# Kernel tuning notes

Hardware: AMD Instinct MI355X
Metric: run time of the kernel (lower is better)

Reference implementation:

```python
import jax, jax.numpy as jnp
import numpy as np

EPS = 1e-8

def _gelu(x):
    return jax.nn.gelu(x, approximate=False)  # torch F.gelu default (erf)

def _film_pool(feat, q, film_w, film_b, hid_w, hid_b, fin_w, fin_b):
    # feat: (B,C,H,W), q: (B,Q,E)
    B, C, H, W = feat.shape
    f = feat.reshape(B, C, H * W).transpose(0, 2, 1)            # (B,HW,C)
    gb = q @ film_w + film_b                                    # (B,Q,2C)
    gamma, beta = jnp.split(gb, 2, axis=-1)                     # (B,Q,C) each
    mod = gamma[:, :, None, :] * f[:, None, :, :] + beta[:, :, None, :]  # (B,Q,HW,C)
    h = _gelu(mod @ hid_w + hid_b)                              # (B,Q,HW,Hh)
    attn = jax.nn.sigmoid(h @ fin_w + fin_b)                    # (B,Q,HW,1)
    pooled = (attn * mod).sum(axis=2) / (attn.sum(axis=2) + EPS)  # (B,Q,C)
    return pooled, attn[..., 0]                                 # attn map (B,Q,HW)

def setup_inputs() -> dict:
    key = jax.random.key(0)
    ks = jax.random.split(key, 32)
    B, Q, E, Hh = 2, 32, 768, 128
    chans = [64, 128, 256]
    hws = [(80, 80), (40, 40), (20, 20)]
    d = {}
    d['feat0'] = jax.random.normal(ks[0], (B, chans[0], *hws[0]), jnp.float32)
    d['feat1'] = jax.random.normal(ks[1], (B, chans[1], *hws[1]), jnp.float32)
    d['feat2'] = jax.random.normal(ks[2], (B, chans[2], *hws[2]), jnp.float32)
    d['fact_embeddings'] = jax.random.normal(ks[3], (B, Q, E), jnp.float32)
    for i, C in enumerate(chans):
        d[f'film_w{i}'] = jax.random.normal(ks[4 + 4 * i], (E, 2 * C), jnp.float32) * 0.02
        d[f'film_b{i}'] = jnp.zeros((2 * C,), jnp.float32)
        d[f'hid_w{i}'] = jax.random.normal(ks[5 + 4 * i], (C, Hh), jnp.float32) * 0.05
        d[f'hid_b{i}'] = jnp.zeros((Hh,), jnp.float32)
        d[f'fin_w{i}'] = jax.random.normal(ks[6 + 4 * i], (Hh, 1), jnp.float32) * 0.05
        d[f'fin_b{i}'] = jnp.zeros((1,), jnp.float32)
    in_dim = sum(chans) + hws[-1][0] * hws[-1][1]  # 448 + 400 = 848
    d['mlp_w1'] = jax.random.normal(ks[20], (in_dim, 512), jnp.float32) * 0.02
    d['mlp_b1'] = jnp.zeros((512,), jnp.float32)
    d['mlp_w2'] = jax.random.normal(ks[21], (512, 256), jnp.float32) * 0.02
    d['mlp_b2'] = jnp.zeros((256,), jnp.float32)
    d['mlp_w3'] = jax.random.normal(ks[22], (256, 1), jnp.float32) * 0.02
    d['mlp_b3'] = jnp.zeros((1,), jnp.float32)
    return d

def reference(feat0, feat1, feat2, fact_embeddings,
              film_w0, film_b0, hid_w0, hid_b0, fin_w0, fin_b0,
              film_w1, film_b1, hid_w1, hid_b1, fin_w1, fin_b1,
              film_w2, film_b2, hid_w2, hid_b2, fin_w2, fin_b2,
              mlp_w1, mlp_b1, mlp_w2, mlp_b2, mlp_w3, mlp_b3):
    q = fact_embeddings
    p0, _ = _film_pool(feat0, q, film_w0, film_b0, hid_w0, hid_b0, fin_w0, fin_b0)
    p1, _ = _film_pool(feat1, q, film_w1, film_b1, hid_w1, hid_b1, fin_w1, fin_b1)
    p2, a2 = _film_pool(feat2, q, film_w2, film_b2, hid_w2, hid_b2, fin_w2, fin_b2)
    cat = jnp.concatenate([p0, p1, p2, a2], axis=2)  # (B,Q,848)
    x = _gelu(cat @ mlp_w1 + mlp_b1)
    x = _gelu(x @ mlp_w2 + mlp_b2)
    logits = (x @ mlp_w3 + mlp_b3)[..., 0]  # (B,Q)
    return logits
```

## Files before the change

kernel.cpp:

```cpp
#include <hip/hip_runtime.h>
#include <math.h>

#define BQ 64
#define HH 128
#define EPS 1e-8f

typedef short bf16x8 __attribute__((ext_vector_type(8)));
typedef float f32x4  __attribute__((ext_vector_type(4)));

__device__ __forceinline__ float gelu_exact(float x) {
    return 0.5f * x * (1.0f + erff(x * 0.70710678118654752440f));
}

__device__ __forceinline__ unsigned bf16_rne(float x) {
    unsigned u = __float_as_uint(x);
    return (u + 0x7FFFu + ((u >> 16) & 1u)) >> 16;
}
__device__ __forceinline__ uint2 split_pack(float a, float b) {
    unsigned ha = bf16_rne(a);
    float fa = __uint_as_float(ha << 16);
    unsigned la = bf16_rne(a - fa);
    unsigned hb = bf16_rne(b);
    float fb = __uint_as_float(hb << 16);
    unsigned lb = bf16_rne(b - fb);
    uint2 r; r.x = ha | (hb << 16); r.y = la | (lb << 16);
    return r;
}

__device__ __forceinline__
void pack_feat_body(int i,
                    const float* __restrict__ f0, const float* __restrict__ f1,
                    const float* __restrict__ f2,
                    unsigned short* __restrict__ p0h, unsigned short* __restrict__ p0l,
                    unsigned short* __restrict__ p1h, unsigned short* __restrict__ p1l,
                    unsigned short* __restrict__ p2h, unsigned short* __restrict__ p2l)
{
    const float* f; unsigned short *oh, *ol; int HW; int idx;
    if (i < 102400)      { f = f0; oh = p0h; ol = p0l; HW = 6400; idx = i; }
    else if (i < 153600) { f = f1; oh = p1h; ol = p1l; HW = 1600; idx = i - 102400; }
    else if (i < 179200) { f = f2; oh = p2h; ol = p2l; HW = 400;  idx = i - 153600; }
    else return;
    const int px = idx % HW;
    const int cgb = idx / HW;
    const float* src = f + ((size_t)cgb * 8) * HW + px;
    float a[8];
    #pragma unroll
    for (int k = 0; k < 8; ++k) a[k] = src[(size_t)k * HW];
    unsigned hwd[4], lwd[4];
    #pragma unroll
    for (int k = 0; k < 4; ++k) {
        uint2 p = split_pack(a[2 * k], a[2 * k + 1]);
        hwd[k] = p.x; lwd[k] = p.y;
    }
    *(uint4*)&oh[(size_t)idx * 8] = make_uint4(hwd[0], hwd[1], hwd[2], hwd[3]);
    *(uint4*)&ol[(size_t)idx * 8] = make_uint4(lwd[0], lwd[1], lwd[2], lwd[3]);
}

__global__ __launch_bounds__(256)
void prep1_kernel(const float* __restrict__ f0, const float* __restrict__ f1,
                  const float* __restrict__ f2,
                  unsigned short* __restrict__ p0h, unsigned short* __restrict__ p0l,
                  unsigned short* __restrict__ p1h, unsigned short* __restrict__ p1l,
                  unsigned short* __restrict__ p2h, unsigned short* __restrict__ p2l,
                  const float* __restrict__ qe,
                  const float* __restrict__ fw0, const float* __restrict__ fb0,
                  const float* __restrict__ fw1, const float* __restrict__ fb1,
                  const float* __restrict__ fw2, const float* __restrict__ fb2,
                  float* __restrict__ gb0, float* __restrict__ gb1, float* __restrict__ gb2)
{
    const int tid = threadIdx.x;
    if (blockIdx.x < 700) {
        pack_feat_body(blockIdx.x * 256 + tid, f0, f1, f2, p0h, p0l, p1h, p1l, p2h, p2l);
        return;
    }
    __shared__ float sq[768];
    __shared__ float sP[256];
    const int bb = blockIdx.x - 700;
    const int chunk = bb >> 6, bq = bb & 63;
    int s, o0;
    if (chunk == 0)      { s = 0; o0 = 0; }
    else if (chunk <= 2) { s = 1; o0 = (chunk - 1) * 128; }
    else                 { s = 2; o0 = (chunk - 3) * 128; }
    const float* fw  = s == 0 ? fw0 : s == 1 ? fw1 : fw2;
    const float* fbv = s == 0 ? fb0 : s == 1 ? fb1 : fb2;
    float* gb        = s == 0 ? gb0 : s == 1 ? gb1 : gb2;
    const int twoC = 128 << s;

    for (int i = tid; i < 768; i += 256) sq[i] = qe[bq * 768 + i];
    __syncthreads();
    const int o = o0 + (tid & 127), half = tid >> 7;
    const int e0 = half * 384;
    float a0 = 0.f, a1 = 0.f;
    #pragma unroll 2
    for (int e = 0; e < 384; e += 2) {
        a0 = fmaf(sq[e0 + e],     fw[(e0 + e) * twoC + o],     a0);
        a1 = fmaf(sq[e0 + e + 1], fw[(e0 + e + 1) * twoC + o], a1);
    }
    sP[tid] = a0 + a1;
    __syncthreads();
    if (tid < 128) {
        int oo = o0 + tid;
        gb[bq * twoC + oo] = sP[tid] + sP[tid + 128] + fbv[oo];
    }
}

__global__ __launch_bounds__(256)
void prep2_kernel(const float* __restrict__ gb0, const float* __restrict__ gb1,
                  const float* __restrict__ gb2,
                  const float* __restrict__ hw0_, const float* __restrict__ hb0,
                  const float* __restrict__ hw1_, const float* __restrict__ hb1,
                  const float* __restrict__ hw2_, const float* __restrict__ hb2,
                  unsigned short* __restrict__ g0h, unsigned short* __restrict__ g0l,
                  unsigned short* __restrict__ g1h, unsigned short* __restrict__ g1l,
                  unsigned short* __restrict__ g2h, unsigned short* __restrict__ g2l,
                  float* __restrict__ b20, float* __restrict__ b21, float* __restrict__ b22)
{
    const int tid = threadIdx.x;
    if (blockIdx.x < 1792) {
        int i = blockIdx.x * 256 + tid;
        const float *gb, *hw; unsigned short *oh, *ol; int C, idx;
        if (i < 65536)       { gb = gb0; hw = hw0_; oh = g0h; ol = g0l; C = 64;  idx = i; }
        else if (i < 196608) { gb = gb1; hw = hw1_; oh = g1h; ol = g1l; C = 128; idx = i - 65536; }
        else                 { gb = gb2; hw = hw2_; oh = g2h; ol = g2l; C = 256; idx = i - 196608; }
        const int j  = idx & 127;
        const int cg = (idx >> 7) % (C / 8);
        const int bq = idx / (128 * (C / 8));
        const int c0 = cg * 8;
        const float* g = gb + bq * 2 * C;
        float a[8];
        #pragma unroll
        for (int k = 0; k < 8; ++k) a[k] = g[c0 + k] * hw[(size_t)(c0 + k) * HH + j];
        unsigned hwd[4], lwd[4];
        #pragma unroll
        for (int k = 0; k < 4; ++k) {
            uint2 p = split_pack(a[2 * k], a[2 * k + 1]);
            hwd[k] = p.x; lwd[k] = p.y;
        }
        *(uint4*)&oh[(size_t)idx * 8] = make_uint4(hwd[0], hwd[1], hwd[2], hwd[3]);
        *(uint4*)&ol[(size_t)idx * 8] = make_uint4(lwd[0], lwd[1], lwd[2], lwd[3]);
        return;
    }
    __shared__ float sBeta[256];
    __shared__ float sP[256];
    const int bb = blockIdx.x - 1792;
    const int s = bb >> 6, bq = bb & 63;
    const float* gb = s == 0 ? gb0 : s == 1 ? gb1 : gb2;
    const float* hw = s == 0 ? hw0_ : s == 1 ? hw1_ : hw2_;
    const float* hb = s == 0 ? hb0 : s == 1 ? hb1 : hb2;
    float* b2       = s == 0 ? b20 : s == 1 ? b21 : b22;
    const int C = 64 << s;

    for (int i = tid; i < C; i += 256) sBeta[i] = gb[bq * 2 * C + C + i];
    __syncthreads();
    const int j = tid & 127, half = tid >> 7;
    const int c0 = half * (C / 2);
    float acc = 0.f;
    for (int c = 0; c < C / 2; ++c)
        acc = fmaf(sBeta[c0 + c], hw[(c0 + c) * HH + j], acc);
    sP[tid] = acc;
    __syncthreads();
    if (tid < 128) b2[bq * HH + tid] = hb[tid] + sP[tid] + sP[tid + 128];
}

#define MFMA3(ACC, ALO, AHI, BH, BL)                                            \
    ACC = __builtin_amdgcn_mfma_f32_16x16x32_bf16(ALO, BH, ACC, 0, 0, 0);       \
    ACC = __builtin_amdgcn_mfma_f32_16x16x32_bf16(AHI, BL, ACC, 0, 0, 0);       \
    ACC = __builtin_amdgcn_mfma_f32_16x16x32_bf16(AHI, BH, ACC, 0, 0, 0);

template<int C, bool WRITE_ATTN>
__device__ __forceinline__
void pool_body(const float* __restrict__ feat, int HW,
               const unsigned short* __restrict__ fh, const unsigned short* __restrict__ fl,
               const unsigned short* __restrict__ gwh, const unsigned short* __restrict__ gwl,
               const float* __restrict__ b2, const float* __restrict__ finw,
               const float* __restrict__ finb,
               float* __restrict__ Sout, float* __restrict__ attn_out,
               int b, int qp, int tile,
               unsigned short* sB, float* sAttn)
{
    const int tid  = threadIdx.x;
    const int w    = tid >> 6;
    const int lane = tid & 63;
    const int l15  = lane & 15, l4 = lane >> 4;
    const int px0  = tile * 256;
    constexpr int CG = C / 8;
    const int bq0 = b * 32 + qp * 2;
    const int bq1 = bq0 + 1;
    const float* fbase = feat + (size_t)b * C * HW;

    f32x4 accA[2][8], accB[2][8];
    #pragma unroll
    for (int jt = 0; jt < 8; ++jt) {
        float bv0 = b2[bq0 * HH + jt * 16 + l15];
        float bv1 = b2[bq1 * HH + jt * 16 + l15];
        accA[0][jt] = (f32x4){bv0, bv0, bv0, bv0};
        accA[1][jt] = (f32x4){bv0, bv0, bv0, bv0};
        accB[0][jt] = (f32x4){bv1, bv1, bv1, bv1};
        accB[1][jt] = (f32x4){bv1, bv1, bv1, bv1};
    }

    const int apx0 = min(px0 + (w * 2 + 0) * 16 + l15, HW - 1);
    const int apx1 = min(px0 + (w * 2 + 1) * 16 + l15, HW - 1);
    const unsigned short* fhp = fh + (size_t)b * CG * HW * 8;
    const unsigned short* flp = fl + (size_t)b * CG * HW * 8;
    const unsigned short* q0h = gwh + (size_t)bq0 * CG * 128 * 8;
    const unsigned short* q0l = gwl + (size_t)bq0 * CG * 128 * 8;
    const unsigned short* q1h = gwh + (size_t)bq1 * CG * 128 * 8;
    const unsigned short* q1l = gwl + (size_t)bq1 * CG * 128 * 8;

    for (int ks = 0; ks < CG / 4; ++ks) {
        const size_t arow = (size_t)(ks * 4 + l4) * HW;
        const bf16x8 Ahi0 = *(const bf16x8*)(fhp + (arow + apx0) * 8);
        const bf16x8 Alo0 = *(const bf16x8*)(flp + (arow + apx0) * 8);
        const bf16x8 Ahi1 = *(const bf16x8*)(fhp + (arow + apx1) * 8);
        const bf16x8 Alo1 = *(const bf16x8*)(flp + (arow + apx1) * 8);
        {
            uint4* dst = (uint4*)sB;
            dst[tid]        = ((const uint4*)(q0h + (size_t)ks * 4096))[tid];
            dst[512  + tid] = ((const uint4*)(q0l + (size_t)ks * 4096))[tid];
            dst[1024 + tid] = ((const uint4*)(q1h + (size_t)ks * 4096))[tid];
            dst[1536 + tid] = ((const uint4*)(q1l + (size_t)ks * 4096))[tid];
        }
        __syncthreads();
        const int bofs = (l4 * 128 + l15) * 8;
        #pragma unroll
        for (int jt = 0; jt < 8; ++jt) {
            const bf16x8 B0h = *(const bf16x8*)(sB + bofs + jt * 128);
            const bf16x8 B0l = *(const bf16x8*)(sB + 4096 + bofs + jt * 128);
            MFMA3(accA[0][jt], Alo0, Ahi0, B0h, B0l)
            MFMA3(accA[1][jt], Alo1, Ahi1, B0h, B0l)
            const bf16x8 B1h = *(const bf16x8*)(sB + 8192 + bofs + jt * 128);
            const bf16x8 B1l = *(const bf16x8*)(sB + 12288 + bofs + jt * 128);
            MFMA3(accB[0][jt], Alo0, Ahi0, B1h, B1l)
            MFMA3(accB[1][jt], Alo1, Ahi1, B1h, B1l)
        }
        __syncthreads();
    }

    const float fb0 = finb[0];
    #pragma unroll
    for (int pt = 0; pt < 2; ++pt) {
        float p0[4] = {0.f, 0.f, 0.f, 0.f};
        float p1[4] = {0.f, 0.f, 0.f, 0.f};
        #pragma unroll
        for (int jt = 0; jt < 8; ++jt) {
            float fwv = finw[jt * 16 + l15];
            #pragma unroll
            for (int r = 0; r < 4; ++r) {
                p0[r] = fmaf(gelu_exact(accA[pt][jt][r]), fwv, p0[r]);
                p1[r] = fmaf(gelu_exact(accB[pt][jt][r]), fwv, p1[r]);
            }
        }
        #pragma unroll
        for (int r = 0; r < 4; ++r) {
            p0[r] += __shfl_xor(p0[r], 1);  p1[r] += __shfl_xor(p1[r], 1);
            p0[r] += __shfl_xor(p0[r], 2);  p1[r] += __shfl_xor(p1[r], 2);
            p0[r] += __shfl_xor(p0[r], 4);  p1[r] += __shfl_xor(p1[r], 4);
            p0[r] += __shfl_xor(p0[r], 8);  p1[r] += __shfl_xor(p1[r], 8);
        }
        if (l15 == 0) {
            #pragma unroll
            for (int r = 0; r < 4; ++r) {
                int lpx = (w * 2 + pt) * 16 + l4 * 4 + r;
                int px  = px0 + lpx;
                float a0v = (px < HW) ? 1.0f / (1.0f + expf(-(p0[r] + fb0))) : 0.0f;
                float a1v = (px < HW) ? 1.0f / (1.0f + expf(-(p1[r] + fb0))) : 0.0f;
                sAttn[lpx]       = a0v;
                sAttn[256 + lpx] = a1v;
                if (WRITE_ATTN && px < HW) {
                    attn_out[bq0 * HW + px] = a0v;
                    attn_out[bq1 * HW + px] = a1v;
                }
            }
        }
    }
    __syncthreads();

    {
        float sa = sAttn[tid];
        #pragma unroll
        for (int d = 1; d < 64; d <<= 1) sa += __shfl_xor(sa, d);
        if (lane == 0) {
            int bqx = (tid < 256) ? bq0 : bq1;
            atomicAdd(&Sout[bqx * (C + 1) + C], sa);
        }
    }

    constexpr int CPW = C / 8;
    #pragma unroll 1
    for (int ci = 0; ci < CPW; ++ci) {
        const int c2 = w * CPW + ci;
        const float* fr = fbase + (size_t)c2 * HW;
        float s0 = 0.f, s1 = 0.f;
        #pragma unroll
        for (int k = 0; k < 4; ++k) {
            int lpx = lane + 64 * k;
            int gc = min(px0 + lpx, HW - 1);
            float fv = fr[gc];
            s0 = fmaf(fv, sAttn[lpx], s0);
            s1 = fmaf(fv, sAttn[256 + lpx], s1);
        }
        #pragma unroll
        for (int d = 1; d < 64; d <<= 1) {
            s0 += __shfl_xor(s0, d);
            s1 += __shfl_xor(s1, d);
        }
        if (lane == 0) {
            atomicAdd(&Sout[bq0 * (C + 1) + c2], s0);
            atomicAdd(&Sout[bq1 * (C + 1) + c2], s1);
        }
    }
}

__global__ __launch_bounds__(512)
void pool_fused(const unsigned short* __restrict__ f0h, const unsigned short* __restrict__ f0l,
                const unsigned short* __restrict__ f1h, const unsigned short* __restrict__ f1l,
                const unsigned short* __restrict__ f2h, const unsigned short* __restrict__ f2l,
                const unsigned short* __restrict__ g0h, const unsigned short* __restrict__ g0l,
                const unsigned short* __restrict__ g1h, const unsigned short* __restrict__ g1l,
                const unsigned short* __restrict__ g2h, const unsigned short* __restrict__ g2l,
                const float* __restrict__ feat0, const float* __restrict__ feat1,
                const float* __restrict__ feat2,
                const float* __restrict__ b20, const float* __restrict__ b21,
                const float* __restrict__ b22,
                const float* __restrict__ finw0, const float* __restrict__ finb0,
                const float* __restrict__ finw1, const float* __restrict__ finb1,
                const float* __restrict__ finw2, const float* __restrict__ finb2,
                float* __restrict__ S0, float* __restrict__ S1, float* __restrict__ S2,
                float* __restrict__ attn2)
{
    __shared__ __align__(16) unsigned short sB[16384];
    __shared__ float sAttn[512];
    const int blk = blockIdx.x;
    if (blk < 64) {
        int bt = blk >> 4, qp = blk & 15;
        int b = bt >> 1, t = bt & 1;
        pool_body<256, true>(feat2, 400, f2h, f2l, g2h, g2l, b22, finw2, finb2,
                             S2, attn2, b, qp, t, sB, sAttn);
    } else if (blk < 288) {
        int bb = blk - 64; int bt = bb >> 4, qp = bb & 15;
        int b = bt / 7, t = bt % 7;
        pool_body<128, false>(feat1, 1600, f1h, f1l, g1h, g1l, b21, finw1, finb1,
                              S1, nullptr, b, qp, t, sB, sAttn);
    } else {
        int bb = blk - 288; int bt = bb >> 4, qp = bb & 15;
        int b = bt / 25, t = bt % 25;
        pool_body<64, false>(feat0, 6400, f0h, f0l, g0h, g0l, b20, finw0, finb0,
                             S0, nullptr, b, qp, t, sB, sAttn);
    }
}

__global__ __launch_bounds__(256)
void mlp1_kernel(const float* __restrict__ S0, const float* __restrict__ S1,
                 const float* __restrict__ S2,
                 const float* __restrict__ gb0, const float* __restrict__ gb1,
                 const float* __restrict__ gb2,
                 const float* __restrict__ attn2,
                 const float* __restrict__ w1, const float* __restrict__ b1,
                 float* __restrict__ X1)
{
    __shared__ float sCat[848];
    __shared__ float sP[256];
    const int tid = threadIdx.x, bq = blockIdx.x;

    for (int i = tid; i < 448; i += 256) {
        int sc, c;
        if (i < 64)       { sc = 0; c = i; }
        else if (i < 192) { sc = 1; c = i - 64; }
        else              { sc = 2; c = i - 192; }
        const int C = 64 << sc;
        const float* So = (sc == 0) ? S0 : (sc == 1) ? S1 : S2;
        const float* g  = (sc == 0) ? gb0 : (sc == 1) ? gb1 : gb2;
        float Sa = So[bq * (C + 1) + C];
        float Sf = So[bq * (C + 1) + c];
        float gamma = g[bq * 2 * C + c];
        float beta  = g[bq * 2 * C + C + c];
        sCat[i] = (gamma * Sf + beta * Sa) / (Sa + EPS);
    }
    for (int i = tid; i < 400; i += 256) sCat[448 + i] = attn2[bq * 400 + i];
    __syncthreads();

    const int o = blockIdx.y * 128 + (tid & 127), half = tid >> 7;
    const int k0 = half * 424;
    float a0 = 0.f, a1 = 0.f;
    #pragma unroll 2
    for (int k = 0; k < 424; k += 2) {
        a0 = fmaf(sCat[k0 + k],     w1[(k0 + k) * 512 + o],     a0);
        a1 = fmaf(sCat[k0 + k + 1], w1[(k0 + k + 1) * 512 + o], a1);
    }
    sP[tid] = a0 + a1;
    __syncthreads();
    if (tid < 128) {
        int oo = blockIdx.y * 128 + tid;
        X1[bq * 512 + oo] = sP[tid] + sP[tid + 128] + b1[oo];
    }
}

__global__ __launch_bounds__(256)
void mlp23_kernel(const float* __restrict__ X1,
                  const float* __restrict__ w2, const float* __restrict__ b2,
                  const float* __restrict__ w3, const float* __restrict__ b3,
                  float* __restrict__ out)
{
    __shared__ float sX1[512];
    __shared__ float sX2[256];
    __shared__ float sR[4];
    const int tid = threadIdx.x, bq = blockIdx.x;
    for (int i = tid; i < 512; i += 256) sX1[i] = gelu_exact(X1[bq * 512 + i]);
    __syncthreads();
    float a0 = b2[tid], a1 = 0.f, a2 = 0.f, a3 = 0.f;
    #pragma unroll 4
    for (int k = 0; k < 512; k += 4) {
        a0 = fmaf(sX1[k],     w2[(k)     * 256 + tid], a0);
        a1 = fmaf(sX1[k + 1], w2[(k + 1) * 256 + tid], a1);
        a2 = fmaf(sX1[k + 2], w2[(k + 2) * 256 + tid], a2);
        a3 = fmaf(sX1[k + 3], w2[(k + 3) * 256 + tid], a3);
    }
    sX2[tid] = gelu_exact((a0 + a1) + (a2 + a3));
    __syncthreads();
    float p = sX2[tid] * w3[tid];
    #pragma unroll
    for (int d = 1; d < 64; d <<= 1) p += __shfl_xor(p, d);
    if ((tid & 63) == 0) sR[tid >> 6] = p;
    __syncthreads();
    if (tid == 0) out[bq] = sR[0] + sR[1] + sR[2] + sR[3] + b3[0];
}

extern "C" void kernel_launch(void* const* d_in, const int* in_sizes, int n_in,
                              void* d_out, int out_size, void* d_ws, size_t ws_size,
                              hipStream_t stream)
{
    const float* feat0 = (const float*)d_in[0];
    const float* feat1 = (const float*)d_in[1];
    const float* feat2 = (const float*)d_in[2];
    const float* qe    = (const float*)d_in[3];
    const float* film_w0 = (const float*)d_in[4];
    const float* film_b0 = (const float*)d_in[5];
    const float* hid_w0  = (const float*)d_in[6];
    const float* hid_b0  = (const float*)d_in[7];
    const float* fin_w0  = (const float*)d_in[8];
    const float* fin_b0  = (const float*)d_in[9];
    const float* film_w1 = (const float*)d_in[10];
    const float* film_b1 = (const float*)d_in[11];
    const float* hid_w1  = (const float*)d_in[12];
    const float* hid_b1  = (const float*)d_in[13];
    const float* fin_w1  = (const float*)d_in[14];
    const float* fin_b1  = (const float*)d_in[15];
    const float* film_w2 = (const float*)d_in[16];
    const float* film_b2 = (const float*)d_in[17];
    const float* hid_w2  = (const float*)d_in[18];
    const float* hid_b2  = (const float*)d_in[19];
    const float* fin_w2  = (const float*)d_in[20];
    const float* fin_b2  = (const float*)d_in[21];
    const float* mlp_w1  = (const float*)d_in[22];
    const float* mlp_b1  = (const float*)d_in[23];
    const float* mlp_w2  = (const float*)d_in[24];
    const float* mlp_b2  = (const float*)d_in[25];
    const float* mlp_w3  = (const float*)d_in[26];
    const float* mlp_b3  = (const float*)d_in[27];

    float* ws = (float*)d_ws;
    float* S0    = ws;
    float* S1    = ws + 4160;
    float* S2    = ws + 12416;
    float* gb0   = ws + 28864;
    float* gb1   = ws + 37056;
    float* gb2   = ws + 53440;
    float* b20   = ws + 86208;
    float* b21   = ws + 94400;
    float* b22   = ws + 102592;
    float* attn2 = ws + 110784;
    float* X1    = ws + 136384;

    unsigned short* us = (unsigned short*)(ws + 169216);
    unsigned short* f0h = us;
    unsigned short* f0l = f0h + 819200;
    unsigned short* f1h = f0l + 819200;
    unsigned short* f1l = f1h + 409600;
    unsigned short* f2h = f1l + 409600;
    unsigned short* f2l = f2h + 204800;
    unsigned short* g0h = f2l + 204800;
    unsigned short* g0l = g0h + 524288;
    unsigned short* g1h = g0l + 524288;
    unsigned short* g1l = g1h + 1048576;
    unsigned short* g2h = g1l + 1048576;
    unsigned short* g2l = g2h + 2097152;

    hipMemsetAsync(d_ws, 0, 28864 * sizeof(float), stream);

    prep1_kernel<<<1148, 256, 0, stream>>>(
        feat0, feat1, feat2, f0h, f0l, f1h, f1l, f2h, f2l,
        qe, film_w0, film_b0, film_w1, film_b1, film_w2, film_b2,
        gb0, gb1, gb2);

    prep2_kernel<<<1984, 256, 0, stream>>>(
        gb0, gb1, gb2,
        hid_w0, hid_b0, hid_w1, hid_b1, hid_w2, hid_b2,
        g0h, g0l, g1h, g1l, g2h, g2l,
        b20, b21, b22);

    pool_fused<<<1088, 512, 0, stream>>>(
        f0h, f0l, f1h, f1l, f2h, f2l,
        g0h, g0l, g1h, g1l, g2h, g2l,
        feat0, feat1, feat2,
        b20, b21, b22,
        fin_w0, fin_b0, fin_w1, fin_b1, fin_w2, fin_b2,
        S0, S1, S2, attn2);

    mlp1_kernel<<<dim3(BQ, 4), 256, 0, stream>>>(
        S0, S1, S2, gb0, gb1, gb2, attn2, mlp_w1, mlp_b1, X1);

    mlp23_kernel<<<BQ, 256, 0, stream>>>(
        X1, mlp_w2, mlp_b2, mlp_w3, mlp_b3, (float*)d_out);
}
```

Before: 233.8 us.

## Double-buffer FiLM weight tiles via direct global-to-LDS loads and XCD-aware block mapping

```diff
diff --git a/kernel.cpp b/kernel.cpp
--- a/kernel.cpp
+++ b/kernel.cpp
@@ -7,6 +7,9 @@
 
 typedef short bf16x8 __attribute__((ext_vector_type(8)));
 typedef float f32x4  __attribute__((ext_vector_type(4)));
+
+typedef const __attribute__((address_space(1))) void* gptr_t;
+typedef __attribute__((address_space(3))) void* lptr_t;
 
 __device__ __forceinline__ float gelu_exact(float x) {
     return 0.5f * x * (1.0f + erff(x * 0.70710678118654752440f));
@@ -183,7 +186,8 @@
     const int lane = tid & 63;
     const int l15  = lane & 15, l4 = lane >> 4;
     const int px0  = tile * 256;
-    constexpr int CG = C / 8;
+    constexpr int CG  = C / 8;
+    constexpr int NKS = CG / 4;
     const int bq0 = b * 32 + qp * 2;
     const int bq1 = bq0 + 1;
     const float* fbase = feat + (size_t)b * C * HW;
@@ -203,39 +207,53 @@
     const int apx1 = min(px0 + (w * 2 + 1) * 16 + l15, HW - 1);
     const unsigned short* fhp = fh + (size_t)b * CG * HW * 8;
     const unsigned short* flp = fl + (size_t)b * CG * HW * 8;
-    const unsigned short* q0h = gwh + (size_t)bq0 * CG * 128 * 8;
-    const unsigned short* q0l = gwl + (size_t)bq0 * CG * 128 * 8;
-    const unsigned short* q1h = gwh + (size_t)bq1 * CG * 128 * 8;
-    const unsigned short* q1l = gwl + (size_t)bq1 * CG * 128 * 8;
-
-    for (int ks = 0; ks < CG / 4; ++ks) {
+    const unsigned short* qsrc0 = gwh + (size_t)bq0 * CG * 1024;
+    const unsigned short* qsrc1 = gwl + (size_t)bq0 * CG * 1024;
+    const unsigned short* qsrc2 = gwh + (size_t)bq1 * CG * 1024;
+    const unsigned short* qsrc3 = gwl + (size_t)bq1 * CG * 1024;
+
+    const int lane8 = lane * 8;
+    const int woff  = __builtin_amdgcn_readfirstlane(w * 512);
+
+    #define STAGE(KS, BUF)                                                       \
+    {                                                                            \
+        const unsigned short* s0 = qsrc0 + (size_t)(KS) * 4096 + woff + lane8;   \
+        const unsigned short* s1 = qsrc1 + (size_t)(KS) * 4096 + woff + lane8;   \
+        const unsigned short* s2 = qsrc2 + (size_t)(KS) * 4096 + woff + lane8;   \
+        const unsigned short* s3 = qsrc3 + (size_t)(KS) * 4096 + woff + lane8;   \
+        __builtin_amdgcn_global_load_lds((gptr_t)s0, (lptr_t)((BUF) + 0    + woff), 16, 0, 0); \
+        __builtin_amdgcn_global_load_lds((gptr_t)s1, (lptr_t)((BUF) + 4096 + woff), 16, 0, 0); \
+        __builtin_amdgcn_global_load_lds((gptr_t)s2, (lptr_t)((BUF) + 8192 + woff), 16, 0, 0); \
+        __builtin_amdgcn_global_load_lds((gptr_t)s3, (lptr_t)((BUF) + 12288 + woff), 16, 0, 0); \
+    }
+
+    STAGE(0, sB)
+
+    for (int ks = 0; ks < NKS; ++ks) {
+        __syncthreads();
+        unsigned short* cur = sB + (ks & 1) * 16384;
+        if (ks + 1 < NKS) STAGE(ks + 1, sB + (((ks + 1) & 1) * 16384))
+
         const size_t arow = (size_t)(ks * 4 + l4) * HW;
         const bf16x8 Ahi0 = *(const bf16x8*)(fhp + (arow + apx0) * 8);
         const bf16x8 Alo0 = *(const bf16x8*)(flp + (arow + apx0) * 8);
         const bf16x8 Ahi1 = *(const bf16x8*)(fhp + (arow + apx1) * 8);
         const bf16x8 Alo1 = *(const bf16x8*)(flp + (arow + apx1) * 8);
-        {
-            uint4* dst = (uint4*)sB;
-            dst[tid]        = ((const uint4*)(q0h + (size_t)ks * 4096))[tid];
-            dst[512  + tid] = ((const uint4*)(q0l + (size_t)ks * 4096))[tid];
-            dst[1024 + tid] = ((const uint4*)(q1h + (size_t)ks * 4096))[tid];
-            dst[1536 + tid] = ((const uint4*)(q1l + (size_t)ks * 4096))[tid];
-        }
-        __syncthreads();
+
         const int bofs = (l4 * 128 + l15) * 8;
         #pragma unroll
         for (int jt = 0; jt < 8; ++jt) {
-            const bf16x8 B0h = *(const bf16x8*)(sB + bofs + jt * 128);
-            const bf16x8 B0l = *(const bf16x8*)(sB + 4096 + bofs + jt * 128);
+            const bf16x8 B0h = *(const bf16x8*)(cur + bofs + jt * 128);
+            const bf16x8 B0l = *(const bf16x8*)(cur + 4096 + bofs + jt * 128);
             MFMA3(accA[0][jt], Alo0, Ahi0, B0h, B0l)
             MFMA3(accA[1][jt], Alo1, Ahi1, B0h, B0l)
-            const bf16x8 B1h = *(const bf16x8*)(sB + 8192 + bofs + jt * 128);
-            const bf16x8 B1l = *(const bf16x8*)(sB + 12288 + bofs + jt * 128);
+            const bf16x8 B1h = *(const bf16x8*)(cur + 8192 + bofs + jt * 128);
+            const bf16x8 B1l = *(const bf16x8*)(cur + 12288 + bofs + jt * 128);
             MFMA3(accB[0][jt], Alo0, Ahi0, B1h, B1l)
             MFMA3(accB[1][jt], Alo1, Ahi1, B1h, B1l)
         }
-        __syncthreads();
-    }
+    }
+    #undef STAGE
 
     const float fb0 = finb[0];
     #pragma unroll
@@ -329,22 +347,26 @@
                 float* __restrict__ S0, float* __restrict__ S1, float* __restrict__ S2,
                 float* __restrict__ attn2)
 {
-    __shared__ __align__(16) unsigned short sB[16384];
-    __shared__ float sAttn[512];
-    const int blk = blockIdx.x;
-    if (blk < 64) {
-        int bt = blk >> 4, qp = blk & 15;
-        int b = bt >> 1, t = bt & 1;
+    __shared__ __align__(16) unsigned short sB[32768];
+    float* sAttn = (float*)sB;
+
+    const int blk0 = blockIdx.x;
+    const int xcd = blk0 & 7, s = blk0 >> 3;
+    int k, t;
+    if (s < 8)       { k = s >> 1;            t = s & 1; }
+    else if (s < 36) { k = 4 + (s - 8) / 7;   t = (s - 8) % 7; }
+    else             { k = 8 + (s - 36) / 25; t = (s - 36) % 25; }
+    const int b  = xcd >> 2;
+    const int qp = (k & 3) * 4 + (xcd & 3);
+    const int sidx = k >> 2;
+
+    if (sidx == 0) {
         pool_body<256, true>(feat2, 400, f2h, f2l, g2h, g2l, b22, finw2, finb2,
                              S2, attn2, b, qp, t, sB, sAttn);
-    } else if (blk < 288) {
-        int bb = blk - 64; int bt = bb >> 4, qp = bb & 15;
-        int b = bt / 7, t = bt % 7;
+    } else if (sidx == 1) {
         pool_body<128, false>(feat1, 1600, f1h, f1l, g1h, g1l, b21, finw1, finb1,
                               S1, nullptr, b, qp, t, sB, sAttn);
     } else {
-        int bb = blk - 288; int bt = bb >> 4, qp = bb & 15;
-        int b = bt / 25, t = bt % 25;
         pool_body<64, false>(feat0, 6400, f0h, f0l, g0h, g0l, b20, finw0, finb0,
                              S0, nullptr, b, qp, t, sB, sAttn);
     }
```

Result: slower. 246.7 us (+5.5%).

## Stage full per-query weights in LDS once and loop pixel tiles per block

Applied to the files above, without the earlier changes.

```diff
diff --git a/kernel.cpp b/kernel.cpp
--- a/kernel.cpp
+++ b/kernel.cpp
@@ -25,6 +25,9 @@
     unsigned lb = bf16_rne(b - fb);
     uint2 r; r.x = ha | (hb << 16); r.y = la | (lb << 16);
     return r;
+}
+__device__ __forceinline__ float bf_to_f(unsigned short u) {
+    return __uint_as_float((unsigned)u << 16);
 }
 
 __device__ __forceinline__
@@ -66,11 +69,17 @@
                   const float* __restrict__ fw0, const float* __restrict__ fb0,
                   const float* __restrict__ fw1, const float* __restrict__ fb1,
                   const float* __restrict__ fw2, const float* __restrict__ fb2,
-                  float* __restrict__ gb0, float* __restrict__ gb1, float* __restrict__ gb2)
+                  float* __restrict__ gb0, float* __restrict__ gb1, float* __restrict__ gb2,
+                  float* __restrict__ zws)
 {
     const int tid = threadIdx.x;
     if (blockIdx.x < 700) {
         pack_feat_body(blockIdx.x * 256 + tid, f0, f1, f2, p0h, p0l, p1h, p1l, p2h, p2l);
+        return;
+    }
+    if (blockIdx.x >= 1148) {
+        int idx = (blockIdx.x - 1148) * 256 + tid;
+        if (idx < 28864) zws[idx] = 0.0f;
         return;
     }
     __shared__ float sq[768];
@@ -167,148 +176,175 @@
     ACC = __builtin_amdgcn_mfma_f32_16x16x32_bf16(AHI, BL, ACC, 0, 0, 0);       \
     ACC = __builtin_amdgcn_mfma_f32_16x16x32_bf16(AHI, BH, ACC, 0, 0, 0);
 
-template<int C, bool WRITE_ATTN>
+template<int C, int QF, bool WRITE_ATTN>
 __device__ __forceinline__
-void pool_body(const float* __restrict__ feat, int HW,
+void pool_body(int HW,
                const unsigned short* __restrict__ fh, const unsigned short* __restrict__ fl,
                const unsigned short* __restrict__ gwh, const unsigned short* __restrict__ gwl,
                const float* __restrict__ b2, const float* __restrict__ finw,
                const float* __restrict__ finb,
                float* __restrict__ Sout, float* __restrict__ attn_out,
-               int b, int qp, int tile,
+               int b, int qidx, int t0, int nt,
                unsigned short* sB, float* sAttn)
 {
     const int tid  = threadIdx.x;
     const int w    = tid >> 6;
     const int lane = tid & 63;
     const int l15  = lane & 15, l4 = lane >> 4;
-    const int px0  = tile * 256;
-    constexpr int CG = C / 8;
-    const int bq0 = b * 32 + qp * 2;
+    constexpr int CG   = C / 8;
+    constexpr int NKS  = CG / 4;
+    constexpr int SLAB = QF * 8192;
+    const int bq0 = b * 32 + qidx * QF;
     const int bq1 = bq0 + 1;
-    const float* fbase = feat + (size_t)b * C * HW;
-
-    f32x4 accA[2][8], accB[2][8];
-    #pragma unroll
-    for (int jt = 0; jt < 8; ++jt) {
-        float bv0 = b2[bq0 * HH + jt * 16 + l15];
-        float bv1 = b2[bq1 * HH + jt * 16 + l15];
-        accA[0][jt] = (f32x4){bv0, bv0, bv0, bv0};
-        accA[1][jt] = (f32x4){bv0, bv0, bv0, bv0};
-        accB[0][jt] = (f32x4){bv1, bv1, bv1, bv1};
-        accB[1][jt] = (f32x4){bv1, bv1, bv1, bv1};
-    }
-
-    const int apx0 = min(px0 + (w * 2 + 0) * 16 + l15, HW - 1);
-    const int apx1 = min(px0 + (w * 2 + 1) * 16 + l15, HW - 1);
+
     const unsigned short* fhp = fh + (size_t)b * CG * HW * 8;
     const unsigned short* flp = fl + (size_t)b * CG * HW * 8;
-    const unsigned short* q0h = gwh + (size_t)bq0 * CG * 128 * 8;
-    const unsigned short* q0l = gwl + (size_t)bq0 * CG * 128 * 8;
-    const unsigned short* q1h = gwh + (size_t)bq1 * CG * 128 * 8;
-    const unsigned short* q1l = gwl + (size_t)bq1 * CG * 128 * 8;
-
-    for (int ks = 0; ks < CG / 4; ++ks) {
-        const size_t arow = (size_t)(ks * 4 + l4) * HW;
-        const bf16x8 Ahi0 = *(const bf16x8*)(fhp + (arow + apx0) * 8);
-        const bf16x8 Alo0 = *(const bf16x8*)(flp + (arow + apx0) * 8);
-        const bf16x8 Ahi1 = *(const bf16x8*)(fhp + (arow + apx1) * 8);
-        const bf16x8 Alo1 = *(const bf16x8*)(flp + (arow + apx1) * 8);
-        {
-            uint4* dst = (uint4*)sB;
-            dst[tid]        = ((const uint4*)(q0h + (size_t)ks * 4096))[tid];
-            dst[512  + tid] = ((const uint4*)(q0l + (size_t)ks * 4096))[tid];
-            dst[1024 + tid] = ((const uint4*)(q1h + (size_t)ks * 4096))[tid];
-            dst[1536 + tid] = ((const uint4*)(q1l + (size_t)ks * 4096))[tid];
-        }
-        __syncthreads();
-        const int bofs = (l4 * 128 + l15) * 8;
+
+    {
+        const unsigned short* srcs[4];
+        srcs[0] = gwh + (size_t)bq0 * CG * 1024;
+        srcs[1] = gwl + (size_t)bq0 * CG * 1024;
+        if (QF == 2) {
+            srcs[2] = gwh + (size_t)bq1 * CG * 1024;
+            srcs[3] = gwl + (size_t)bq1 * CG * 1024;
+        }
+        #pragma unroll
+        for (int ks = 0; ks < NKS; ++ks) {
+            #pragma unroll
+            for (int p = 0; p < 2 * QF; ++p) {
+                const uint4* s = (const uint4*)(srcs[p] + (size_t)ks * 4096);
+                uint4* d = (uint4*)(sB + ks * SLAB + p * 4096);
+                d[tid] = s[tid];
+            }
+        }
+    }
+    __syncthreads();
+
+    const float fb0 = finb[0];
+
+    for (int ti = 0; ti < nt; ++ti) {
+        const int tile = t0 + ti;
+        const int px0  = tile * 256;
+        const int apx0 = min(px0 + (w * 2 + 0) * 16 + l15, HW - 1);
+        const int apx1 = min(px0 + (w * 2 + 1) * 16 + l15, HW - 1);
+
+        f32x4 accA[2][8], accB[2][8];
         #pragma unroll
         for (int jt = 0; jt < 8; ++jt) {
-            const bf16x8 B0h = *(const bf16x8*)(sB + bofs + jt * 128);
-            const bf16x8 B0l = *(const bf16x8*)(sB + 4096 + bofs + jt * 128);
-            MFMA3(accA[0][jt], Alo0, Ahi0, B0h, B0l)
-            MFMA3(accA[1][jt], Alo1, Ahi1, B0h, B0l)
-            const bf16x8 B1h = *(const bf16x8*)(sB + 8192 + bofs + jt * 128);
-            const bf16x8 B1l = *(const bf16x8*)(sB + 12288 + bofs + jt * 128);
-            MFMA3(accB[0][jt], Alo0, Ahi0, B1h, B1l)
-            MFMA3(accB[1][jt], Alo1, Ahi1, B1h, B1l)
+            float bv0 = b2[bq0 * HH + jt * 16 + l15];
+            accA[0][jt] = (f32x4){bv0, bv0, bv0, bv0};
+            accA[1][jt] = (f32x4){bv0, bv0, bv0, bv0};
+            if (QF == 2) {
+                float bv1 = b2[bq1 * HH + jt * 16 + l15];
+                accB[0][jt] = (f32x4){bv1, bv1, bv1, bv1};
+                accB[1][jt] = (f32x4){bv1, bv1, bv1, bv1};
+            }
+        }
+
+        #pragma unroll 2
+        for (int ks = 0; ks < NKS; ++ks) {
+            const size_t ar = (size_t)(ks * 4 + l4) * HW;
+            const bf16x8 Ahi0 = *(const bf16x8*)(fhp + (ar + apx0) * 8);
+            const bf16x8 Alo0 = *(const bf16x8*)(flp + (ar + apx0) * 8);
+            const bf16x8 Ahi1 = *(const bf16x8*)(fhp + (ar + apx1) * 8);
+            const bf16x8 Alo1 = *(const bf16x8*)(flp + (ar + apx1) * 8);
+            const unsigned short* S = sB + ks * SLAB;
+            const int bofs = (l4 * 128 + l15) * 8;
+            #pragma unroll
+            for (int jt = 0; jt < 8; ++jt) {
+                const bf16x8 B0h = *(const bf16x8*)(S + bofs + jt * 128);
+                const bf16x8 B0l = *(const bf16x8*)(S + 4096 + bofs + jt * 128);
+                MFMA3(accA[0][jt], Alo0, Ahi0, B0h, B0l)
+                MFMA3(accA[1][jt], Alo1, Ahi1, B0h, B0l)
+                if (QF == 2) {
+                    const bf16x8 B1h = *(const bf16x8*)(S + 8192 + bofs + jt * 128);
+                    const bf16x8 B1l = *(const bf16x8*)(S + 12288 + bofs + jt * 128);
+                    MFMA3(accB[0][jt], Alo0, Ahi0, B1h, B1l)
+                    MFMA3(accB[1][jt], Alo1, Ahi1, B1h, B1l)
+                }
+            }
+        }
+
+        #pragma unroll
+        for (int pt = 0; pt < 2; ++pt) {
+            float p0[4] = {0.f, 0.f, 0.f, 0.f};
+            float p1[4] = {0.f, 0.f, 0.f, 0.f};
+            #pragma unroll
+            for (int jt = 0; jt < 8; ++jt) {
+                float fwv = finw[jt * 16 + l15];
+                #pragma unroll
+                for (int r = 0; r < 4; ++r) {
+                    p0[r] = fmaf(gelu_exact(accA[pt][jt][r]), fwv, p0[r]);
+                    if (QF == 2) p1[r] = fmaf(gelu_exact(accB[pt][jt][r]), fwv, p1[r]);
+                }
+            }
+            #pragma unroll
+            for (int r = 0; r < 4; ++r) {
+                p0[r] += __shfl_xor(p0[r], 1);
+                p0[r] += __shfl_xor(p0[r], 2);
+                p0[r] += __shfl_xor(p0[r], 4);
+                p0[r] += __shfl_xor(p0[r], 8);
+                if (QF == 2) {
+                    p1[r] += __shfl_xor(p1[r], 1);
+                    p1[r] += __shfl_xor(p1[r], 2);
+                    p1[r] += __shfl_xor(p1[r], 4);
+                    p1[r] += __shfl_xor(p1[r], 8);
+                }
+            }
+            if (l15 == 0) {
+                #pragma unroll
+                for (int r = 0; r < 4; ++r) {
+                    int lpx = (w * 2 + pt) * 16 + l4 * 4 + r;
+                    int px  = px0 + lpx;
+                    float a0v = (px < HW) ? 1.0f / (1.0f + expf(-(p0[r] + fb0))) : 0.0f;
+                    sAttn[lpx] = a0v;
+                    if (WRITE_ATTN && px < HW) attn_out[bq0 * HW + px] = a0v;
+                    if (QF == 2) {
+                        float a1v = (px < HW) ? 1.0f / (1.0f + expf(-(p1[r] + fb0))) : 0.0f;
+                        sAttn[256 + lpx] = a1v;
+                        if (WRITE_ATTN && px < HW) attn_out[bq1 * HW + px] = a1v;
+                    }
+                }
+            }
         }
         __syncthreads();
-    }
-
-    const float fb0 = finb[0];
-    #pragma unroll
-    for (int pt = 0; pt < 2; ++pt) {
-        float p0[4] = {0.f, 0.f, 0.f, 0.f};
-        float p1[4] = {0.f, 0.f, 0.f, 0.f};
-        #pragma unroll
-        for (int jt = 0; jt < 8; ++jt) {
-            float fwv = finw[jt * 16 + l15];
-            #pragma unroll
-            for (int r = 0; r < 4; ++r) {
-                p0[r] = fmaf(gelu_exact(accA[pt][jt][r]), fwv, p0[r]);
-                p1[r] = fmaf(gelu_exact(accB[pt][jt][r]), fwv, p1[r]);
-            }
-        }
-        #pragma unroll
-        for (int r = 0; r < 4; ++r) {
-            p0[r] += __shfl_xor(p0[r], 1);  p1[r] += __shfl_xor(p1[r], 1);
-            p0[r] += __shfl_xor(p0[r], 2);  p1[r] += __shfl_xor(p1[r], 2);
-            p0[r] += __shfl_xor(p0[r], 4);  p1[r] += __shfl_xor(p1[r], 4);
-            p0[r] += __shfl_xor(p0[r], 8);  p1[r] += __shfl_xor(p1[r], 8);
-        }
-        if (l15 == 0) {
-            #pragma unroll
-            for (int r = 0; r < 4; ++r) {
-                int lpx = (w * 2 + pt) * 16 + l4 * 4 + r;
-                int px  = px0 + lpx;
-                float a0v = (px < HW) ? 1.0f / (1.0f + expf(-(p0[r] + fb0))) : 0.0f;
-                float a1v = (px < HW) ? 1.0f / (1.0f + expf(-(p1[r] + fb0))) : 0.0f;
-                sAttn[lpx]       = a0v;
-                sAttn[256 + lpx] = a1v;
-                if (WRITE_ATTN && px < HW) {
-                    attn_out[bq0 * HW + px] = a0v;
-                    attn_out[bq1 * HW + px] = a1v;
-                }
-            }
-        }
-    }
-    __syncthreads();
-
-    {
-        float sa = sAttn[tid];
-        #pragma unroll
-        for (int d = 1; d < 64; d <<= 1) sa += __shfl_xor(sa, d);
-        if (lane == 0) {
-            int bqx = (tid < 256) ? bq0 : bq1;
-            atomicAdd(&Sout[bqx * (C + 1) + C], sa);
-        }
-    }
-
-    constexpr int CPW = C / 8;
-    #pragma unroll 1
-    for (int ci = 0; ci < CPW; ++ci) {
-        const int c2 = w * CPW + ci;
-        const float* fr = fbase + (size_t)c2 * HW;
-        float s0 = 0.f, s1 = 0.f;
-        #pragma unroll
-        for (int k = 0; k < 4; ++k) {
-            int lpx = lane + 64 * k;
-            int gc = min(px0 + lpx, HW - 1);
-            float fv = fr[gc];
-            s0 = fmaf(fv, sAttn[lpx], s0);
-            s1 = fmaf(fv, sAttn[256 + lpx], s1);
-        }
-        #pragma unroll
-        for (int d = 1; d < 64; d <<= 1) {
-            s0 += __shfl_xor(s0, d);
-            s1 += __shfl_xor(s1, d);
-        }
-        if (lane == 0) {
-            atomicAdd(&Sout[bq0 * (C + 1) + c2], s0);
-            atomicAdd(&Sout[bq1 * (C + 1) + c2], s1);
-        }
+
+        if (QF == 2 || tid < 256) {
+            float sa = sAttn[tid];
+            #pragma unroll
+            for (int d = 1; d < 64; d <<= 1) sa += __shfl_xor(sa, d);
+            if (lane == 0) {
+                int bqx = (tid < 256) ? bq0 : bq1;
+                atomicAdd(&Sout[bqx * (C + 1) + C], sa);
+            }
+        }
+
+        constexpr int CPW = C / 8;
+        #pragma unroll 1
+        for (int ci = 0; ci < CPW; ++ci) {
+            const int c2 = w * CPW + ci;
+            const unsigned short* ph = fhp + ((size_t)(c2 >> 3) * HW) * 8 + (c2 & 7);
+            const unsigned short* pl = flp + ((size_t)(c2 >> 3) * HW) * 8 + (c2 & 7);
+            float s0 = 0.f, s1 = 0.f;
+            #pragma unroll
+            for (int k = 0; k < 4; ++k) {
+                int lpx = lane + 64 * k;
+                int gc = min(px0 + lpx, HW - 1);
+                float fv = bf_to_f(ph[(size_t)gc * 8]) + bf_to_f(pl[(size_t)gc * 8]);
+                s0 = fmaf(fv, sAttn[lpx], s0);
+                if (QF == 2) s1 = fmaf(fv, sAttn[256 + lpx], s1);
+            }
+            #pragma unroll
+            for (int d = 1; d < 64; d <<= 1) {
+                s0 += __shfl_xor(s0, d);
+                if (QF == 2) s1 += __shfl_xor(s1, d);
+            }
+            if (lane == 0) {
+                atomicAdd(&Sout[bq0 * (C + 1) + c2], s0);
+                if (QF == 2) atomicAdd(&Sout[bq1 * (C + 1) + c2], s1);
+            }
+        }
+        __syncthreads();
     }
 }
 
@@ -319,8 +355,6 @@
                 const unsigned short* __restrict__ g0h, const unsigned short* __restrict__ g0l,
                 const unsigned short* __restrict__ g1h, const unsigned short* __restrict__ g1l,
                 const unsigned short* __restrict__ g2h, const unsigned short* __restrict__ g2l,
-                const float* __restrict__ feat0, const float* __restrict__ feat1,
-                const float* __restrict__ feat2,
                 const float* __restrict__ b20, const float* __restrict__ b21,
                 const float* __restrict__ b22,
                 const float* __restrict__ finw0, const float* __restrict__ finb0,
@@ -329,24 +363,30 @@
                 float* __restrict__ S0, float* __restrict__ S1, float* __restrict__ S2,
                 float* __restrict__ attn2)
 {
-    __shared__ __align__(16) unsigned short sB[16384];
+    __shared__ __align__(16) unsigned short sB[65536];
     __shared__ float sAttn[512];
     const int blk = blockIdx.x;
-    if (blk < 64) {
-        int bt = blk >> 4, qp = blk & 15;
-        int b = bt >> 1, t = bt & 1;
-        pool_body<256, true>(feat2, 400, f2h, f2l, g2h, g2l, b22, finw2, finb2,
-                             S2, attn2, b, qp, t, sB, sAttn);
-    } else if (blk < 288) {
-        int bb = blk - 64; int bt = bb >> 4, qp = bb & 15;
-        int b = bt / 7, t = bt % 7;
-        pool_body<128, false>(feat1, 1600, f1h, f1l, g1h, g1l, b21, finw1, finb1,
-                              S1, nullptr, b, qp, t, sB, sAttn);
+    if (blk < 128) {
+        int bb = blk;
+        int b = bb >> 6, r = bb & 63;
+        int qp = r >> 2, tq = r & 3;
+        int t0 = (tq == 0) ? 0 : 7 + (tq - 1) * 6;
+        int nt = (tq == 0) ? 7 : 6;
+        pool_body<64, 2, false>(6400, f0h, f0l, g0h, g0l, b20, finw0, finb0,
+                                S0, nullptr, b, qp, t0, nt, sB, sAttn);
+    } else if (blk < 192) {
+        int bb = blk - 128;
+        int b = bb >> 5, r = bb & 31;
+        int qp = r >> 1, tq = r & 1;
+        int t0 = tq ? 4 : 0;
+        int nt = tq ? 3 : 4;
+        pool_body<128, 2, false>(1600, f1h, f1l, g1h, g1l, b21, finw1, finb1,
+                                 S1, nullptr, b, qp, t0, nt, sB, sAttn);
     } else {
-        int bb = blk - 288; int bt = bb >> 4, qp = bb & 15;
-        int b = bt / 25, t = bt % 25;
-        pool_body<64, false>(feat0, 6400, f0h, f0l, g0h, g0l, b20, finw0, finb0,
-                             S0, nullptr, b, qp, t, sB, sAttn);
+        int bb = blk - 192;
+        int b = bb >> 5, q = bb & 31;
+        pool_body<256, 1, true>(400, f2h, f2l, g2h, g2l, b22, finw2, finb2,
+                                S2, attn2, b, q, 0, 2, sB, sAttn);
     }
 }
 
@@ -486,12 +526,10 @@
     unsigned short* g2h = g1l + 1048576;
     unsigned short* g2l = g2h + 2097152;
 
-    hipMemsetAsync(d_ws, 0, 28864 * sizeof(float), stream);
-
-    prep1_kernel<<<1148, 256, 0, stream>>>(
+    prep1_kernel<<<1261, 256, 0, stream>>>(
         feat0, feat1, feat2, f0h, f0l, f1h, f1l, f2h, f2l,
         qe, film_w0, film_b0, film_w1, film_b1, film_w2, film_b2,
-        gb0, gb1, gb2);
+        gb0, gb1, gb2, ws);
 
     prep2_kernel<<<1984, 256, 0, stream>>>(
         gb0, gb1, gb2,
@@ -499,10 +537,9 @@
         g0h, g0l, g1h, g1l, g2h, g2l,
         b20, b21, b22);
 
-    pool_fused<<<1088, 512, 0, stream>>>(
+    pool_fused<<<256, 512, 0, stream>>>(
         f0h, f0l, f1h, f1l, f2h, f2l,
         g0h, g0l, g1h, g1l, g2h, g2l,
-        feat0, feat1, feat2,
         b20, b21, b22,
         fin_w0, fin_b0, fin_w1, fin_b1, fin_w2, fin_b2,
         S0, S1, S2, attn2);
```

After: 316.2 us. +35.3%, slower.

## Batch FiLM GEMV over queries, pre-transpose hid_w, fold memset, reuse packed feats

Applied to the files above, without the earlier changes.

```diff
diff --git a/kernel.cpp b/kernel.cpp
--- a/kernel.cpp
+++ b/kernel.cpp
@@ -25,6 +25,9 @@
     unsigned lb = bf16_rne(b - fb);
     uint2 r; r.x = ha | (hb << 16); r.y = la | (lb << 16);
     return r;
+}
+__device__ __forceinline__ float bf_to_f(unsigned short u) {
+    return __uint_as_float((unsigned)u << 16);
 }
 
 __device__ __forceinline__
@@ -66,42 +69,72 @@
                   const float* __restrict__ fw0, const float* __restrict__ fb0,
                   const float* __restrict__ fw1, const float* __restrict__ fb1,
                   const float* __restrict__ fw2, const float* __restrict__ fb2,
-                  float* __restrict__ gb0, float* __restrict__ gb1, float* __restrict__ gb2)
+                  const float* __restrict__ hw0_, const float* __restrict__ hw1_,
+                  const float* __restrict__ hw2_,
+                  float* __restrict__ gb0, float* __restrict__ gb1, float* __restrict__ gb2,
+                  float* __restrict__ hwT0, float* __restrict__ hwT1, float* __restrict__ hwT2,
+                  float* __restrict__ zws)
 {
     const int tid = threadIdx.x;
-    if (blockIdx.x < 700) {
-        pack_feat_body(blockIdx.x * 256 + tid, f0, f1, f2, p0h, p0l, p1h, p1l, p2h, p2l);
+    const int blk = blockIdx.x;
+    if (blk < 700) {
+        pack_feat_body(blk * 256 + tid, f0, f1, f2, p0h, p0l, p1h, p1l, p2h, p2l);
         return;
     }
-    __shared__ float sq[768];
-    __shared__ float sP[256];
-    const int bb = blockIdx.x - 700;
-    const int chunk = bb >> 6, bq = bb & 63;
-    int s, o0;
-    if (chunk == 0)      { s = 0; o0 = 0; }
-    else if (chunk <= 2) { s = 1; o0 = (chunk - 1) * 128; }
-    else                 { s = 2; o0 = (chunk - 3) * 128; }
-    const float* fw  = s == 0 ? fw0 : s == 1 ? fw1 : fw2;
-    const float* fbv = s == 0 ? fb0 : s == 1 ? fb1 : fb2;
-    float* gb        = s == 0 ? gb0 : s == 1 ? gb1 : gb2;
-    const int twoC = 128 << s;
-
-    for (int i = tid; i < 768; i += 256) sq[i] = qe[bq * 768 + i];
-    __syncthreads();
-    const int o = o0 + (tid & 127), half = tid >> 7;
-    const int e0 = half * 384;
-    float a0 = 0.f, a1 = 0.f;
-    #pragma unroll 2
-    for (int e = 0; e < 384; e += 2) {
-        a0 = fmaf(sq[e0 + e],     fw[(e0 + e) * twoC + o],     a0);
-        a1 = fmaf(sq[e0 + e + 1], fw[(e0 + e + 1) * twoC + o], a1);
-    }
-    sP[tid] = a0 + a1;
-    __syncthreads();
-    if (tid < 128) {
-        int oo = o0 + tid;
-        gb[bq * twoC + oo] = sP[tid] + sP[tid + 128] + fbv[oo];
-    }
+    if (blk < 756) {
+        __shared__ float sq8[8 * 768];
+        const int bb = blk - 700;
+        const int chunk = bb >> 3, grp = bb & 7;
+        int s, o0;
+        if (chunk == 0)      { s = 0; o0 = 0; }
+        else if (chunk <= 2) { s = 1; o0 = (chunk - 1) * 128; }
+        else                 { s = 2; o0 = (chunk - 3) * 128; }
+        const float* fw  = s == 0 ? fw0 : s == 1 ? fw1 : fw2;
+        const float* fbv = s == 0 ? fb0 : s == 1 ? fb1 : fb2;
+        float* gb        = s == 0 ? gb0 : s == 1 ? gb1 : gb2;
+        const int twoC = 128 << s;
+        const int bq0 = grp * 8;
+
+        for (int i = tid; i < 8 * 768; i += 256)
+            sq8[i] = qe[(bq0 + i / 768) * 768 + (i % 768)];
+        __syncthreads();
+
+        const int o = o0 + (tid & 127);
+        const int qh = (tid >> 7) * 4;
+        float a0 = 0.f, a1 = 0.f, a2 = 0.f, a3 = 0.f;
+        #pragma unroll 2
+        for (int e = 0; e < 768; ++e) {
+            const float fwv = fw[(size_t)e * twoC + o];
+            a0 = fmaf(fwv, sq8[(qh + 0) * 768 + e], a0);
+            a1 = fmaf(fwv, sq8[(qh + 1) * 768 + e], a1);
+            a2 = fmaf(fwv, sq8[(qh + 2) * 768 + e], a2);
+            a3 = fmaf(fwv, sq8[(qh + 3) * 768 + e], a3);
+        }
+        const float fbb = fbv[o];
+        gb[(bq0 + qh + 0) * twoC + o] = a0 + fbb;
+        gb[(bq0 + qh + 1) * twoC + o] = a1 + fbb;
+        gb[(bq0 + qh + 2) * twoC + o] = a2 + fbb;
+        gb[(bq0 + qh + 3) * twoC + o] = a3 + fbb;
+        return;
+    }
+    if (blk < 784) {
+        int i = (blk - 756) * 256 + tid;
+        const float* hw; float* dst; int idx;
+        if (i < 1024)      { hw = hw0_; dst = hwT0; idx = i; }
+        else if (i < 3072) { hw = hw1_; dst = hwT1; idx = i - 1024; }
+        else if (i < 7168) { hw = hw2_; dst = hwT2; idx = i - 3072; }
+        else return;
+        const int j = idx & 127, cg = idx >> 7;
+        float a[8];
+        #pragma unroll
+        for (int k = 0; k < 8; ++k) a[k] = hw[(size_t)(cg * 8 + k) * 128 + j];
+        float4* d = (float4*)(dst + (size_t)idx * 8);
+        d[0] = make_float4(a[0], a[1], a[2], a[3]);
+        d[1] = make_float4(a[4], a[5], a[6], a[7]);
+        return;
+    }
+    int idx = (blk - 784) * 256 + tid;
+    if (idx < 28864) zws[idx] = 0.0f;
 }
 
 __global__ __launch_bounds__(256)
@@ -110,6 +143,8 @@
                   const float* __restrict__ hw0_, const float* __restrict__ hb0,
                   const float* __restrict__ hw1_, const float* __restrict__ hb1,
                   const float* __restrict__ hw2_, const float* __restrict__ hb2,
+                  const float* __restrict__ hwT0, const float* __restrict__ hwT1,
+                  const float* __restrict__ hwT2,
                   unsigned short* __restrict__ g0h, unsigned short* __restrict__ g0l,
                   unsigned short* __restrict__ g1h, unsigned short* __restrict__ g1l,
                   unsigned short* __restrict__ g2h, unsigned short* __restrict__ g2l,
@@ -118,18 +153,22 @@
     const int tid = threadIdx.x;
     if (blockIdx.x < 1792) {
         int i = blockIdx.x * 256 + tid;
-        const float *gb, *hw; unsigned short *oh, *ol; int C, idx;
-        if (i < 65536)       { gb = gb0; hw = hw0_; oh = g0h; ol = g0l; C = 64;  idx = i; }
-        else if (i < 196608) { gb = gb1; hw = hw1_; oh = g1h; ol = g1l; C = 128; idx = i - 65536; }
-        else                 { gb = gb2; hw = hw2_; oh = g2h; ol = g2l; C = 256; idx = i - 196608; }
+        const float *gb, *hwT; unsigned short *oh, *ol; int C, idx;
+        if (i < 65536)       { gb = gb0; hwT = hwT0; oh = g0h; ol = g0l; C = 64;  idx = i; }
+        else if (i < 196608) { gb = gb1; hwT = hwT1; oh = g1h; ol = g1l; C = 128; idx = i - 65536; }
+        else                 { gb = gb2; hwT = hwT2; oh = g2h; ol = g2l; C = 256; idx = i - 196608; }
         const int j  = idx & 127;
         const int cg = (idx >> 7) % (C / 8);
         const int bq = idx / (128 * (C / 8));
         const int c0 = cg * 8;
         const float* g = gb + bq * 2 * C;
+        const float4* tp = (const float4*)(hwT + ((size_t)cg * 128 + j) * 8);
+        const float4 h0 = tp[0], h1 = tp[1];
+        const float4 g0 = *(const float4*)(g + c0);
+        const float4 g1 = *(const float4*)(g + c0 + 4);
         float a[8];
-        #pragma unroll
-        for (int k = 0; k < 8; ++k) a[k] = g[c0 + k] * hw[(size_t)(c0 + k) * HH + j];
+        a[0] = g0.x * h0.x; a[1] = g0.y * h0.y; a[2] = g0.z * h0.z; a[3] = g0.w * h0.w;
+        a[4] = g1.x * h1.x; a[5] = g1.y * h1.y; a[6] = g1.z * h1.z; a[7] = g1.w * h1.w;
         unsigned hwd[4], lwd[4];
         #pragma unroll
         for (int k = 0; k < 4; ++k) {
@@ -169,7 +208,7 @@
 
 template<int C, bool WRITE_ATTN>
 __device__ __forceinline__
-void pool_body(const float* __restrict__ feat, int HW,
+void pool_body(int HW,
                const unsigned short* __restrict__ fh, const unsigned short* __restrict__ fl,
                const unsigned short* __restrict__ gwh, const unsigned short* __restrict__ gwl,
                const float* __restrict__ b2, const float* __restrict__ finw,
@@ -186,7 +225,6 @@
     constexpr int CG = C / 8;
     const int bq0 = b * 32 + qp * 2;
     const int bq1 = bq0 + 1;
-    const float* fbase = feat + (size_t)b * C * HW;
 
     f32x4 accA[2][8], accB[2][8];
     #pragma unroll
@@ -203,10 +241,10 @@
     const int apx1 = min(px0 + (w * 2 + 1) * 16 + l15, HW - 1);
     const unsigned short* fhp = fh + (size_t)b * CG * HW * 8;
     const unsigned short* flp = fl + (size_t)b * CG * HW * 8;
-    const unsigned short* q0h = gwh + (size_t)bq0 * CG * 128 * 8;
-    const unsigned short* q0l = gwl + (size_t)bq0 * CG * 128 * 8;
-    const unsigned short* q1h = gwh + (size_t)bq1 * CG * 128 * 8;
-    const unsigned short* q1l = gwl + (size_t)bq1 * CG * 128 * 8;
+    const unsigned short* q0h = gwh + (size_t)bq0 * CG * 1024;
+    const unsigned short* q0l = gwl + (size_t)bq0 * CG * 1024;
+    const unsigned short* q1h = gwh + (size_t)bq1 * CG * 1024;
+    const unsigned short* q1l = gwl + (size_t)bq1 * CG * 1024;
 
     for (int ks = 0; ks < CG / 4; ++ks) {
         const size_t arow = (size_t)(ks * 4 + l4) * HW;
@@ -290,13 +328,14 @@
     #pragma unroll 1
     for (int ci = 0; ci < CPW; ++ci) {
         const int c2 = w * CPW + ci;
-        const float* fr = fbase + (size_t)c2 * HW;
+        const unsigned short* ph = fhp + ((size_t)(c2 >> 3) * HW) * 8 + (c2 & 7);
+        const unsigned short* pl = flp + ((size_t)(c2 >> 3) * HW) * 8 + (c2 & 7);
         float s0 = 0.f, s1 = 0.f;
         #pragma unroll
         for (int k = 0; k < 4; ++k) {
             int lpx = lane + 64 * k;
             int gc = min(px0 + lpx, HW - 1);
-            float fv = fr[gc];
+            float fv = bf_to_f(ph[(size_t)gc * 8]) + bf_to_f(pl[(size_t)gc * 8]);
             s0 = fmaf(fv, sAttn[lpx], s0);
             s1 = fmaf(fv, sAttn[256 + lpx], s1);
         }
@@ -319,8 +358,6 @@
                 const unsigned short* __restrict__ g0h, const unsigned short* __restrict__ g0l,
                 const unsigned short* __restrict__ g1h, const unsigned short* __restrict__ g1l,
                 const unsigned short* __restrict__ g2h, const unsigned short* __restrict__ g2l,
-                const float* __restrict__ feat0, const float* __restrict__ feat1,
-                const float* __restrict__ feat2,
                 const float* __restrict__ b20, const float* __restrict__ b21,
                 const float* __restrict__ b22,
                 const float* __restrict__ finw0, const float* __restrict__ finb0,
@@ -335,17 +372,17 @@
     if (blk < 64) {
         int bt = blk >> 4, qp = blk & 15;
         int b = bt >> 1, t = bt & 1;
-        pool_body<256, true>(feat2, 400, f2h, f2l, g2h, g2l, b22, finw2, finb2,
+        pool_body<256, true>(400, f2h, f2l, g2h, g2l, b22, finw2, finb2,
                              S2, attn2, b, qp, t, sB, sAttn);
     } else if (blk < 288) {
         int bb = blk - 64; int bt = bb >> 4, qp = bb & 15;
         int b = bt / 7, t = bt % 7;
-        pool_body<128, false>(feat1, 1600, f1h, f1l, g1h, g1l, b21, finw1, finb1,
+        pool_body<128, false>(1600, f1h, f1l, g1h, g1l, b21, finw1, finb1,
                               S1, nullptr, b, qp, t, sB, sAttn);
     } else {
         int bb = blk - 288; int bt = bb >> 4, qp = bb & 15;
         int b = bt / 25, t = bt % 25;
-        pool_body<64, false>(feat0, 6400, f0h, f0l, g0h, g0l, b20, finw0, finb0,
+        pool_body<64, false>(6400, f0h, f0l, g0h, g0l, b20, finw0, finb0,
                              S0, nullptr, b, qp, t, sB, sAttn);
     }
 }
@@ -485,24 +522,26 @@
     unsigned short* g1l = g1h + 1048576;
     unsigned short* g2h = g1l + 1048576;
     unsigned short* g2l = g2h + 2097152;
-
-    hipMemsetAsync(d_ws, 0, 28864 * sizeof(float), stream);
-
-    prep1_kernel<<<1148, 256, 0, stream>>>(
+    float* hwT0 = ws + 169216 + 5103616;
+    float* hwT1 = hwT0 + 8192;
+    float* hwT2 = hwT1 + 16384;
+
+    prep1_kernel<<<897, 256, 0, stream>>>(
         feat0, feat1, feat2, f0h, f0l, f1h, f1l, f2h, f2l,
         qe, film_w0, film_b0, film_w1, film_b1, film_w2, film_b2,
-        gb0, gb1, gb2);
+        hid_w0, hid_w1, hid_w2,
+        gb0, gb1, gb2, hwT0, hwT1, hwT2, ws);
 
     prep2_kernel<<<1984, 256, 0, stream>>>(
         gb0, gb1, gb2,
         hid_w0, hid_b0, hid_w1, hid_b1, hid_w2, hid_b2,
+        hwT0, hwT1, hwT2,
         g0h, g0l, g1h, g1l, g2h, g2l,
         b20, b21, b22);
 
     pool_fused<<<1088, 512, 0, stream>>>(
         f0h, f0l, f1h, f1l, f2h, f2l,
         g0h, g0l, g1h, g1l, g2h, g2l,
-        feat0, feat1, feat2,
         b20, b21, b22,
         fin_w0, fin_b0, fin_w1, fin_b1, fin_w2, fin_b2,
         S0, S1, S2, attn2);
```

Result: slower. 326.7 us (+39.7%).
